# Optimization experiments

Hardware: AMD Instinct MI355X
Metric: run time of the kernel (lower is better)

The kernel has to match this reference:

```python
import jax, jax.numpy as jnp
import numpy as np

BS, NQ, DIM, HEADS, POINTS, LEVELS = 2, 4096, 768, 6, 4, 1
HD = DIM // HEADS
H = W = 64
NV = H * W
EPS = 1e-6


def setup_inputs() -> dict:
    key = jax.random.key(0)
    ks = jax.random.split(key, 16)
    s = 0.02  # param init scale
    return {
        "query": jax.random.normal(ks[0], (BS, NQ, DIM), jnp.float32),
        "reference_points": jax.random.uniform(ks[1], (BS, NQ, LEVELS, 2), jnp.float32),
        "feat": jax.random.normal(ks[2], (BS, NV, DIM), jnp.float32),
        "spatial_shapes": np.array([[H, W]], dtype=np.int64),
        "level_start_index": np.array([0], dtype=np.int64),
        "ln_w": jnp.ones((DIM,), jnp.float32),
        "ln_b": jnp.zeros((DIM,), jnp.float32),
        "vp_w": jax.random.normal(ks[3], (DIM, DIM), jnp.float32) * s,
        "vp_b": jnp.zeros((DIM,), jnp.float32),
        "off_w": jax.random.normal(ks[4], (DIM, HEADS * LEVELS * POINTS * 2), jnp.float32) * s,
        "off_b": jax.random.normal(ks[5], (HEADS * LEVELS * POINTS * 2,), jnp.float32),
        "aw_w": jax.random.normal(ks[6], (DIM, HEADS * LEVELS * POINTS), jnp.float32) * s,
        "aw_b": jnp.zeros((HEADS * LEVELS * POINTS,), jnp.float32),
        "out_w": jax.random.normal(ks[7], (DIM, DIM), jnp.float32) * s,
        "out_b": jnp.zeros((DIM,), jnp.float32),
        "gamma": jax.random.normal(ks[8], (DIM,), jnp.float32) * 0.1,
    }


def _layernorm(x, w, b):
    mu = jnp.mean(x, axis=-1, keepdims=True)
    var = jnp.mean(jnp.square(x - mu), axis=-1, keepdims=True)
    return (x - mu) * jax.lax.rsqrt(var + EPS) * w + b


def _bilinear_sample(img, loc):
    # img: (bs, heads, H, W, hd); loc: (bs, nq, heads, points, 2) in [0,1]
    # matches torch.grid_sample(align_corners=False, padding_mode='zeros')
    bs, heads, h, w, hd = img.shape
    x = loc[..., 0] * w - 0.5
    y = loc[..., 1] * h - 0.5
    x0 = jnp.floor(x)
    y0 = jnp.floor(y)
    wx = x - x0
    wy = y - y0
    x0i = x0.astype(jnp.int32)
    y0i = y0.astype(jnp.int32)
    bi = jnp.arange(bs)[:, None, None, None]
    hi = jnp.arange(heads)[None, None, :, None]

    def gather(yi, xi):
        valid = (xi >= 0) & (xi < w) & (yi >= 0) & (yi < h)
        v = img[bi, hi, jnp.clip(yi, 0, h - 1), jnp.clip(xi, 0, w - 1)]
        return v * valid[..., None].astype(img.dtype)

    v00 = gather(y0i, x0i)
    v01 = gather(y0i, x0i + 1)
    v10 = gather(y0i + 1, x0i)
    v11 = gather(y0i + 1, x0i + 1)
    wx = wx[..., None]
    wy = wy[..., None]
    return (v00 * (1 - wy) * (1 - wx) + v01 * (1 - wy) * wx
            + v10 * wy * (1 - wx) + v11 * wy * wx)


def _msda(q, value, reference_points, spatial_shapes, off_w, off_b, aw_w, aw_b, out_w, out_b):
    bs, nq, _ = q.shape
    nv = value.shape[1]
    value = value.reshape(bs, nv, HEADS, HD)
    offsets = (q @ off_w + off_b).reshape(bs, nq, HEADS, LEVELS, POINTS, 2)
    aw = jax.nn.softmax(q @ aw_w + aw_b, axis=-1).reshape(bs, nq, HEADS, LEVELS, POINTS)
    # offset_normalizer = [W_l, H_l] per level
    norm = jnp.asarray(np.asarray(spatial_shapes)[:, ::-1], jnp.float32)  # (L, 2)
    loc = reference_points[:, :, None, :, None, :] + offsets / norm[None, None, None, :, None, :]
    # loc: (bs, nq, heads, levels, points, 2)
    out = jnp.zeros((bs, nq, HEADS, HD), jnp.float32)
    start = 0
    for l in range(LEVELS):
        h_l, w_l = int(spatial_shapes[l][0]), int(spatial_shapes[l][1])
        img = value[:, start:start + h_l * w_l].reshape(bs, h_l, w_l, HEADS, HD).transpose(0, 3, 1, 2, 4)
        sampled = _bilinear_sample(img, loc[:, :, :, l])  # (bs, nq, heads, points, hd)
        out = out + jnp.einsum('bnhpd,bnhp->bnhd', sampled, aw[:, :, :, l])
        start += h_l * w_l
    return out.reshape(bs, nq, DIM) @ out_w + out_b


def reference(query, reference_points, feat, spatial_shapes, level_start_index,
              ln_w, ln_b, vp_w, vp_b, off_w, off_b, aw_w, aw_b, out_w, out_b, gamma):
    q = _layernorm(query, ln_w, ln_b)
    value = feat @ vp_w + vp_b
    attn = _msda(q, value, reference_points, spatial_shapes,
                 off_w, off_b, aw_w, aw_b, out_w, out_b)
    # identity = zeros, dropout = 0 -> attn as-is; residual scale by gamma
    return query + gamma * attn
```

## Files before the change

kernel.cpp:

```cpp
#include <hip/hip_runtime.h>
#include <hip/hip_bf16.h>
#include <math.h>

#define BSZ 2
#define NQ 4096
#define DIM 768
#define HEADS 6
#define POINTS 4
#define HD 128
#define HW_DIM 64
#define NV (HW_DIM*HW_DIM)
#define M_TOTAL (BSZ*NQ)
#define KDIM 768
#define KSPLIT 2
#define KPART (KDIM/KSPLIT)

#define BM 64
#define BN 128
#define BKK 64
#define NBLK_M (M_TOTAL/BM)
#define NBLK_N (DIM/BN)
#define GEMM_GRID (NBLK_M*NBLK_N)
#define LN_BLOCKS (M_TOTAL/4)
#define TR_BLOCKS (576+576+72)
#define SMALL_BLOCKS (128*KSPLIT)

#define A_TILE (BM*BKK)
#define B_TILE (BN*BKK)
#define SMEM_U16 (2*(A_TILE+B_TILE))

typedef __attribute__((ext_vector_type(8))) short bf16x8;
typedef __attribute__((ext_vector_type(4))) float f32x4;
typedef unsigned int u32;
typedef unsigned short u16;

__device__ inline u16 f2bf(float f) {
    union { float f; u32 u; } v; v.f = f;
    u32 r = v.u + 0x7fffu + ((v.u >> 16) & 1u);
    return (u16)(r >> 16);
}

#define GLD16(g, l) __builtin_amdgcn_global_load_lds( \
    (const __attribute__((address_space(1))) u32*)(g), \
    (__attribute__((address_space(3))) u32*)(l), 16, 0, 0)

__global__ __launch_bounds__(256) void prep_kernel(
        const float* __restrict__ x, const float* __restrict__ lnw,
        const float* __restrict__ lnb, u16* __restrict__ q,
        const float* __restrict__ feat, u16* __restrict__ feat_bf,
        const float* __restrict__ vp_w,  u16* __restrict__ vp_wt,
        const float* __restrict__ out_w, u16* __restrict__ out_wt,
        const float* __restrict__ off_w, const float* __restrict__ aw_w,
        u16* __restrict__ oaw_wt) {
    int b = blockIdx.x;
    if (b < LN_BLOCKS) {
        int wave = threadIdx.x >> 6, lane = threadIdx.x & 63;
        int row = b * 4 + wave;
        int c = lane * 4;
        const float* xr = x + (size_t)row * DIM;
        const float* fr = feat + (size_t)row * DIM;
        float4 v0 = *(const float4*)(xr + c);
        float4 v1 = *(const float4*)(xr + c + 256);
        float4 v2 = *(const float4*)(xr + c + 512);
        float4 f0 = *(const float4*)(fr + c);
        float4 f1 = *(const float4*)(fr + c + 256);
        float4 f2 = *(const float4*)(fr + c + 512);
        u16* fb = feat_bf + (size_t)row * DIM;
        ushort4 fo;
        fo.x = f2bf(f0.x); fo.y = f2bf(f0.y); fo.z = f2bf(f0.z); fo.w = f2bf(f0.w);
        *(ushort4*)(fb + c) = fo;
        fo.x = f2bf(f1.x); fo.y = f2bf(f1.y); fo.z = f2bf(f1.z); fo.w = f2bf(f1.w);
        *(ushort4*)(fb + c + 256) = fo;
        fo.x = f2bf(f2.x); fo.y = f2bf(f2.y); fo.z = f2bf(f2.z); fo.w = f2bf(f2.w);
        *(ushort4*)(fb + c + 512) = fo;

        float s  = v0.x+v0.y+v0.z+v0.w + v1.x+v1.y+v1.z+v1.w + v2.x+v2.y+v2.z+v2.w;
        float ss = v0.x*v0.x+v0.y*v0.y+v0.z*v0.z+v0.w*v0.w
                 + v1.x*v1.x+v1.y*v1.y+v1.z*v1.z+v1.w*v1.w
                 + v2.x*v2.x+v2.y*v2.y+v2.z*v2.z+v2.w*v2.w;
        #pragma unroll
        for (int st = 1; st < 64; st <<= 1) {
            s  += __shfl_xor(s,  st, 64);
            ss += __shfl_xor(ss, st, 64);
        }
        float mean = s * (1.0f / DIM);
        float var  = ss * (1.0f / DIM) - mean * mean;
        float rstd = rsqrtf(var + 1e-6f);
        u16* qr = q + (size_t)row * DIM;
        #pragma unroll
        for (int g = 0; g < 3; g++) {
            float4 v = (g == 0) ? v0 : (g == 1) ? v1 : v2;
            int cc = c + g * 256;
            const float4 ww = *(const float4*)(lnw + cc);
            const float4 bb = *(const float4*)(lnb + cc);
            ushort4 o;
            o.x = f2bf((v.x - mean) * rstd * ww.x + bb.x);
            o.y = f2bf((v.y - mean) * rstd * ww.y + bb.y);
            o.z = f2bf((v.z - mean) * rstd * ww.z + bb.z);
            o.w = f2bf((v.w - mean) * rstd * ww.w + bb.w);
            *(ushort4*)(qr + cc) = o;
        }
    } else {
        int t = b - LN_BLOCKS;
        int z, xk, yk;
        if (t < 576)      { z = 0; xk = t % 24; yk = t / 24; }
        else if (t < 1152){ z = 1; t -= 576; xk = t % 24; yk = t / 24; }
        else              { z = 2; t -= 1152; xk = t % 3; yk = t / 3; }
        __shared__ float tile[32][33];
        int n0 = xk * 32, k0 = yk * 32;
        int tx = threadIdx.x & 31, ty = threadIdx.x >> 5;
        const float* src = (z == 0) ? vp_w : (z == 1) ? out_w : nullptr;
        u16* dst = (z == 0) ? vp_wt : (z == 1) ? out_wt : oaw_wt;
        #pragma unroll
        for (int r = 0; r < 4; r++) {
            int k = k0 + ty + r * 8, n = n0 + tx;
            float v = 0.0f;
            if (z < 2) {
                v = src[(size_t)k * DIM + n];
            } else {
                if (n < 48) v = off_w[(size_t)k * 48 + n];
                else if (n < 72) v = aw_w[(size_t)k * 24 + (n - 48)];
            }
            tile[ty + r * 8][tx] = v;
        }
        __syncthreads();
        #pragma unroll
        for (int r = 0; r < 4; r++) {
            int nn = ty + r * 8, kk = tx;
            int drow = n0 + nn;
            if (z == 2 && drow >= 80) continue;
            dst[(size_t)drow * KDIM + k0 + kk] = f2bf(tile[kk][nn]);
        }
    }
}

__device__ __forceinline__ void gemm_big_body(int b, u16* __restrict__ smem,
        const u16* __restrict__ A, const u16* __restrict__ Bt,
        const float* __restrict__ bias, void* __restrict__ Cout,
        int storeBF16, const float* __restrict__ resid,
        const float* __restrict__ gamma) {
    u16* As = smem;
    u16* Bs = smem + 2 * A_TILE;
    int tid = threadIdx.x, w = tid >> 6, lane = tid & 63;
    int lm = lane & 15, quad = lane >> 4;
    int xcd = b & 7, idx = b >> 3;
    int mb = xcd * 16 + idx / NBLK_N;
    int nb = idx % NBLK_N;
    int m0 = mb * BM, n0 = nb * BN;
    int wr = w & 1, wc = w >> 1;

    int srow = lane >> 3;
    int scol = (lane & 7) ^ srow;
    const u16* Ab = A + (size_t)m0 * KDIM;
    const u16* Bb = Bt + (size_t)n0 * KDIM;

    f32x4 acc[2][4];
    #pragma unroll
    for (int i = 0; i < 2; i++)
        #pragma unroll
        for (int j = 0; j < 4; j++) acc[i][j] = (f32x4){0.f, 0.f, 0.f, 0.f};

    int aoff[2][2], boff[4][2];
    #pragma unroll
    for (int i = 0; i < 2; i++) {
        int row = wr * 32 + i * 16 + lm;
        #pragma unroll
        for (int kk = 0; kk < 2; kk++)
            aoff[i][kk] = row * BKK + (((quad + 4 * kk) ^ (row & 7)) << 3);
    }
    #pragma unroll
    for (int j = 0; j < 4; j++) {
        int row = wc * 64 + j * 16 + lm;
        #pragma unroll
        for (int kk = 0; kk < 2; kk++)
            boff[j][kk] = row * BKK + (((quad + 4 * kk) ^ (row & 7)) << 3);
    }

    auto stage = [&](int buf, int k0) {
        #pragma unroll
        for (int r = 0; r < 2; r++) {
            int row = r * 32 + w * 8 + srow;
            GLD16(Ab + (size_t)row * KDIM + k0 + scol * 8,
                  As + buf * A_TILE + (r * 32 + w * 8) * BKK);
        }
        #pragma unroll
        for (int r = 0; r < 4; r++) {
            int row = r * 32 + w * 8 + srow;
            GLD16(Bb + (size_t)row * KDIM + k0 + scol * 8,
                  Bs + buf * B_TILE + (r * 32 + w * 8) * BKK);
        }
    };

    stage(0, 0);
    __syncthreads();
    const int NT = KDIM / BKK;
    for (int t = 0; t < NT; t++) {
        if (t + 1 < NT) stage((t + 1) & 1, (t + 1) * BKK);
        const u16* Ap = As + (t & 1) * A_TILE;
        const u16* Bp = Bs + (t & 1) * B_TILE;
        #pragma unroll
        for (int kk = 0; kk < 2; kk++) {
            bf16x8 af[2], bf[4];
            #pragma unroll
            for (int i = 0; i < 2; i++) af[i] = *(const bf16x8*)(Ap + aoff[i][kk]);
            #pragma unroll
            for (int j = 0; j < 4; j++) bf[j] = *(const bf16x8*)(Bp + boff[j][kk]);
            #pragma unroll
            for (int i = 0; i < 2; i++)
                #pragma unroll
                for (int j = 0; j < 4; j++)
                    acc[i][j] = __builtin_amdgcn_mfma_f32_16x16x32_bf16(af[i], bf[j], acc[i][j], 0, 0, 0);
        }
        __syncthreads();
    }

    #pragma unroll
    for (int j = 0; j < 4; j++) {
        int col = n0 + wc * 64 + j * 16 + lm;
        float bb = bias[col];
        #pragma unroll
        for (int i = 0; i < 2; i++) {
            #pragma unroll
            for (int r = 0; r < 4; r++) {
                int row = m0 + wr * 32 + i * 16 + quad * 4 + r;
                size_t idxo = (size_t)row * DIM + col;
                float v = acc[i][j][r] + bb;
                if (storeBF16) {
                    ((u16*)Cout)[idxo] = f2bf(v);
                } else {
                    ((float*)Cout)[idxo] = resid[idxo] + gamma[col] * v;
                }
            }
        }
    }
}

#define SA_TILE (64*32)
#define SB_TILE (80*32)
__device__ __forceinline__ void gemm_small_body(int mblk, int part,
        u16* __restrict__ smem,
        const u16* __restrict__ A, const u16* __restrict__ Bt,
        const float* __restrict__ b0, const float* __restrict__ b1,
        float* __restrict__ C) {
    u16* As2 = smem;
    u16* Bs2 = smem + 2 * SA_TILE;
    int tid = threadIdx.x, wave = tid >> 6, lane = tid & 63;
    int lm = lane & 15, quad = lane >> 4;
    int m0 = mblk * 64;
    int kbase = part * KPART;
    f32x4 acc[5];
    #pragma unroll
    for (int i = 0; i < 5; i++) acc[i] = (f32x4){0.f, 0.f, 0.f, 0.f};
    int lrow = lane >> 2, lcol = (lane & 3) * 8;

    auto stage = [&](int buf, int k0) {
        for (int c = wave; c < 9; c += 4) {
            if (c < 4) {
                GLD16(A + (size_t)(m0 + c * 16 + lrow) * KDIM + k0 + lcol,
                      As2 + buf * SA_TILE + c * 16 * 32);
            } else {
                GLD16(Bt + (size_t)((c - 4) * 16 + lrow) * KDIM + k0 + lcol,
                      Bs2 + buf * SB_TILE + (c - 4) * 16 * 32);
            }
        }
    };

    stage(0, kbase);
    __syncthreads();
    const int NT = KPART / 32;
    for (int t = 0; t < NT; t++) {
        if (t + 1 < NT) stage((t + 1) & 1, kbase + (t + 1) * 32);
        const u16* Ap = As2 + (t & 1) * SA_TILE;
        const u16* Bp = Bs2 + (t & 1) * SB_TILE;
        bf16x8 af = *(const bf16x8*)(Ap + (wave * 16 + lm) * 32 + quad * 8);
        #pragma unroll
        for (int bn = 0; bn < 5; bn++) {
            bf16x8 bv = *(const bf16x8*)(Bp + (bn * 16 + lm) * 32 + quad * 8);
            acc[bn] = __builtin_amdgcn_mfma_f32_16x16x32_bf16(af, bv, acc[bn], 0, 0, 0);
        }
        __syncthreads();
    }
    float* Cp = C + (size_t)part * M_TOTAL * 80;
    #pragma unroll
    for (int bn = 0; bn < 5; bn++) {
        int col = bn * 16 + lm;
        float bb = 0.0f;
        if (part == 0) bb = (col < 48) ? b0[col] : ((col < 72) ? b1[col - 48] : 0.0f);
        #pragma unroll
        for (int r = 0; r < 4; r++) {
            int row = m0 + wave * 16 + quad * 4 + r;
            Cp[(size_t)row * 80 + col] = acc[bn][r] + bb;
        }
    }
}

__global__ __launch_bounds__(256, 3) void gemms_kernel(
        const u16* __restrict__ feat_bf, const u16* __restrict__ vp_wt,
        const float* __restrict__ vp_b, u16* __restrict__ v_bf,
        const u16* __restrict__ q_bf, const u16* __restrict__ oaw_wt,
        const float* __restrict__ off_b, const float* __restrict__ aw_b,
        float* __restrict__ oa) {
    __shared__ __align__(16) u16 smem[SMEM_U16];
    int b = blockIdx.x;
    if (b < SMALL_BLOCKS) {
        gemm_small_body(b & 127, b >> 7, smem, q_bf, oaw_wt, off_b, aw_b, oa);
    } else {
        gemm_big_body(b - SMALL_BLOCKS, smem, feat_bf, vp_wt, vp_b, v_bf, 1,
                      nullptr, nullptr);
    }
}

__global__ __launch_bounds__(256, 3) void outgemm_kernel(
        const u16* __restrict__ s_bf, const u16* __restrict__ out_wt,
        const float* __restrict__ out_b, float* __restrict__ out_f,
        const float* __restrict__ query, const float* __restrict__ gamma) {
    __shared__ __align__(16) u16 smem[SMEM_U16];
    gemm_big_body(blockIdx.x, smem, s_bf, out_wt, out_b, out_f, 0, query, gamma);
}

__global__ __launch_bounds__(192) void sample_kernel(
        const float* __restrict__ oa, const float* __restrict__ refp,
        const u16* __restrict__ v, u16* __restrict__ out) {
    int row = blockIdx.x;
    int b = row >> 12;
    int tid = threadIdx.x;
    __shared__ float s_w[4][24];
    __shared__ int   s_o[4][24];
    __shared__ float s_e[24];
    if (tid < 24) {
        int h = tid >> 2, p = tid & 3;
        float ox = 0.f, oy = 0.f, lg = 0.f;
        #pragma unroll
        for (int part = 0; part < KSPLIT; part++) {
            const float* pp = oa + (size_t)part * M_TOTAL * 80 + (size_t)row * 80;
            ox += pp[h * 8 + p * 2 + 0];
            oy += pp[h * 8 + p * 2 + 1];
            lg += pp[48 + tid];
        }
        float rx = refp[row * 2 + 0], ry = refp[row * 2 + 1];
        float x = (rx + ox * (1.0f / HW_DIM)) * HW_DIM - 0.5f;
        float y = (ry + oy * (1.0f / HW_DIM)) * HW_DIM - 0.5f;
        float fx = floorf(x), fy = floorf(y);
        int x0 = (int)fx, y0 = (int)fy;
        int x1 = x0 + 1, y1 = y0 + 1;
        float wx = x - fx, wy = y - fy;
        float vx0 = (x0 >= 0 && x0 < HW_DIM) ? 1.f : 0.f;
        float vx1 = (x1 >= 0 && x1 < HW_DIM) ? 1.f : 0.f;
        float vy0 = (y0 >= 0 && y0 < HW_DIM) ? 1.f : 0.f;
        float vy1 = (y1 >= 0 && y1 < HW_DIM) ? 1.f : 0.f;
        int xc0 = min(max(x0, 0), HW_DIM - 1), xc1 = min(max(x1, 0), HW_DIM - 1);
        int yc0 = min(max(y0, 0), HW_DIM - 1), yc1 = min(max(y1, 0), HW_DIM - 1);
        int base = b * NV * DIM;
        s_o[0][tid] = base + (yc0 * HW_DIM + xc0) * DIM;
        s_o[1][tid] = base + (yc0 * HW_DIM + xc1) * DIM;
        s_o[2][tid] = base + (yc1 * HW_DIM + xc0) * DIM;
        s_o[3][tid] = base + (yc1 * HW_DIM + xc1) * DIM;
        s_w[0][tid] = (1.f - wy) * (1.f - wx) * vy0 * vx0;
        s_w[1][tid] = (1.f - wy) * wx * vy0 * vx1;
        s_w[2][tid] = wy * (1.f - wx) * vy1 * vx0;
        s_w[3][tid] = wy * wx * vy1 * vx1;
        s_e[tid] = lg;
        float m = s_e[0];
        #pragma unroll
        for (int i = 1; i < 24; i++) m = fmaxf(m, s_e[i]);
        s_e[tid] = expf(lg - m);
    }
    __syncthreads();
    float ssum = 0.0f;
    #pragma unroll
    for (int i = 0; i < 24; i++) ssum += s_e[i];
    float inv = 1.0f / ssum;

    int h = tid >> 5;
    int d4 = (tid & 31) * 4;
    const u16* vb = v + h * HD + d4;
    float a0 = 0.f, a1 = 0.f, a2 = 0.f, a3 = 0.f;
    #pragma unroll
    for (int p = 0; p < 4; p++) {
        int idx = h * 4 + p;
        float aw = s_e[idx] * inv;
        #pragma unroll
        for (int c = 0; c < 4; c++) {
            uint2 u = *(const uint2*)(vb + s_o[c][idx]);
            float w = aw * s_w[c][idx];
            a0 += w * __uint_as_float(u.x << 16);
            a1 += w * __uint_as_float(u.x & 0xffff0000u);
            a2 += w * __uint_as_float(u.y << 16);
            a3 += w * __uint_as_float(u.y & 0xffff0000u);
        }
    }
    uint2 pack;
    pack.x = (u32)f2bf(a0) | ((u32)f2bf(a1) << 16);
    pack.y = (u32)f2bf(a2) | ((u32)f2bf(a3) << 16);
    *(uint2*)&out[(size_t)row * DIM + h * HD + d4] = pack;
}

extern "C" void kernel_launch(void* const* d_in, const int* in_sizes, int n_in,
                              void* d_out, int out_size, void* d_ws, size_t ws_size,
                              hipStream_t stream) {
    const float* query = (const float*)d_in[0];
    const float* refp  = (const float*)d_in[1];
    const float* feat  = (const float*)d_in[2];
    const float* ln_w  = (const float*)d_in[5];
    const float* ln_b  = (const float*)d_in[6];
    const float* vp_w  = (const float*)d_in[7];
    const float* vp_b  = (const float*)d_in[8];
    const float* off_w = (const float*)d_in[9];
    const float* off_b = (const float*)d_in[10];
    const float* aw_w  = (const float*)d_in[11];
    const float* aw_b  = (const float*)d_in[12];
    const float* out_w = (const float*)d_in[13];
    const float* out_b = (const float*)d_in[14];
    const float* gamma = (const float*)d_in[15];

    const size_t MD = (size_t)M_TOTAL * DIM;
    char* ws = (char*)d_ws;
    u16* q_bf    = (u16*)ws;                 ws += MD * 2;
    u16* feat_bf = (u16*)ws;                 ws += MD * 2;
    u16* v_bf    = (u16*)ws;                 ws += MD * 2;
    u16* s_bf    = (u16*)ws;                 ws += MD * 2;
    u16* vp_wt   = (u16*)ws;                 ws += (size_t)DIM * DIM * 2;
    u16* out_wt  = (u16*)ws;                 ws += (size_t)DIM * DIM * 2;
    u16* oaw_wt  = (u16*)ws;                 ws += (size_t)80 * KDIM * 2;
    float* oa    = (float*)ws;               ws += (size_t)KSPLIT * M_TOTAL * 80 * 4;
    float* out_f = (float*)d_out;

    prep_kernel<<<LN_BLOCKS + TR_BLOCKS, 256, 0, stream>>>(
        query, ln_w, ln_b, q_bf, feat, feat_bf,
        vp_w, vp_wt, out_w, out_wt, off_w, aw_w, oaw_wt);
    gemms_kernel<<<SMALL_BLOCKS + GEMM_GRID, 256, 0, stream>>>(
        feat_bf, vp_wt, vp_b, v_bf, q_bf, oaw_wt, off_b, aw_b, oa);
    sample_kernel<<<M_TOTAL, 192, 0, stream>>>(oa, refp, v_bf, s_bf);
    outgemm_kernel<<<GEMM_GRID, 256, 0, stream>>>(s_bf, out_wt, out_b, out_f, query, gamma);
}
```

Measured before the change: 176.3 us.

## Triple-buffer GEMM K-loop with BK=32 and explicit vmcnt waits

Restructures the big GEMM main loop from double buffering with BK=64 to triple buffering with BK=32. Loads run two stages ahead, and each iteration uses a single barrier gated by explicit s_waitcnt vmcnt counts instead of two __syncthreads. The LDS swizzle is reworked for the 4-slot rows, and launch bounds rise to 4 blocks per CU. The aim is to hide global-to-LDS latency and cut barrier overhead, at the cost of more K iterations, each with only half the MFMA work. The small GEMM shares the smem buffer and the BKK macro, which risks side effects there.

```diff
diff --git a/kernel.cpp b/kernel.cpp
--- a/kernel.cpp
+++ b/kernel.cpp
@@ -17,7 +17,7 @@
 
 #define BM 64
 #define BN 128
-#define BKK 64
+#define BKK 32
 #define NBLK_M (M_TOTAL/BM)
 #define NBLK_N (DIM/BN)
 #define GEMM_GRID (NBLK_M*NBLK_N)
@@ -27,7 +27,7 @@
 
 #define A_TILE (BM*BKK)
 #define B_TILE (BN*BKK)
-#define SMEM_U16 (2*(A_TILE+B_TILE))
+#define SMEM_U16 (3*(A_TILE+B_TILE))
 
 typedef __attribute__((ext_vector_type(8))) short bf16x8;
 typedef __attribute__((ext_vector_type(4))) float f32x4;
@@ -140,7 +140,7 @@
         int storeBF16, const float* __restrict__ resid,
         const float* __restrict__ gamma) {
     u16* As = smem;
-    u16* Bs = smem + 2 * A_TILE;
+    u16* Bs = smem + 3 * A_TILE;
     int tid = threadIdx.x, w = tid >> 6, lane = tid & 63;
     int lm = lane & 15, quad = lane >> 4;
     int xcd = b & 7, idx = b >> 3;
@@ -149,8 +149,8 @@
     int m0 = mb * BM, n0 = nb * BN;
     int wr = w & 1, wc = w >> 1;
 
-    int srow = lane >> 3;
-    int scol = (lane & 7) ^ srow;
+    int srow = lane >> 2;
+    int sslot = lane & 3;
     const u16* Ab = A + (size_t)m0 * KDIM;
     const u16* Bb = Bt + (size_t)n0 * KDIM;
 
@@ -160,58 +160,59 @@
         #pragma unroll
         for (int j = 0; j < 4; j++) acc[i][j] = (f32x4){0.f, 0.f, 0.f, 0.f};
 
-    int aoff[2][2], boff[4][2];
+    int aoff[2], boff[4];
     #pragma unroll
     for (int i = 0; i < 2; i++) {
         int row = wr * 32 + i * 16 + lm;
-        #pragma unroll
-        for (int kk = 0; kk < 2; kk++)
-            aoff[i][kk] = row * BKK + (((quad + 4 * kk) ^ (row & 7)) << 3);
+        aoff[i] = row * BKK + ((quad ^ (row & 3)) << 3);
     }
     #pragma unroll
     for (int j = 0; j < 4; j++) {
         int row = wc * 64 + j * 16 + lm;
-        #pragma unroll
-        for (int kk = 0; kk < 2; kk++)
-            boff[j][kk] = row * BKK + (((quad + 4 * kk) ^ (row & 7)) << 3);
+        boff[j] = row * BKK + ((quad ^ (row & 3)) << 3);
     }
 
     auto stage = [&](int buf, int k0) {
+        {
+            int row = w * 16 + srow;
+            int sc = sslot ^ (row & 3);
+            GLD16(Ab + (size_t)row * KDIM + k0 + sc * 8,
+                  As + buf * A_TILE + (w * 16) * BKK);
+        }
         #pragma unroll
         for (int r = 0; r < 2; r++) {
-            int row = r * 32 + w * 8 + srow;
-            GLD16(Ab + (size_t)row * KDIM + k0 + scol * 8,
-                  As + buf * A_TILE + (r * 32 + w * 8) * BKK);
-        }
-        #pragma unroll
-        for (int r = 0; r < 4; r++) {
-            int row = r * 32 + w * 8 + srow;
-            GLD16(Bb + (size_t)row * KDIM + k0 + scol * 8,
-                  Bs + buf * B_TILE + (r * 32 + w * 8) * BKK);
+            int row = r * 64 + w * 16 + srow;
+            int sc = sslot ^ (row & 3);
+            GLD16(Bb + (size_t)row * KDIM + k0 + sc * 8,
+                  Bs + buf * B_TILE + (r * 64 + w * 16) * BKK);
         }
     };
 
+    const int NT = KDIM / BKK;
     stage(0, 0);
-    __syncthreads();
-    const int NT = KDIM / BKK;
+    stage(1, BKK);
     for (int t = 0; t < NT; t++) {
-        if (t + 1 < NT) stage((t + 1) & 1, (t + 1) * BKK);
-        const u16* Ap = As + (t & 1) * A_TILE;
-        const u16* Bp = Bs + (t & 1) * B_TILE;
-        #pragma unroll
-        for (int kk = 0; kk < 2; kk++) {
-            bf16x8 af[2], bf[4];
+        if (t < NT - 1) {
+            asm volatile("s_waitcnt vmcnt(3) lgkmcnt(0)" ::: "memory");
+        } else {
+            asm volatile("s_waitcnt vmcnt(0) lgkmcnt(0)" ::: "memory");
+        }
+        __builtin_amdgcn_sched_barrier(0);
+        __builtin_amdgcn_s_barrier();
+        __builtin_amdgcn_sched_barrier(0);
+        if (t + 2 < NT) stage((t + 2) % 3, (t + 2) * BKK);
+        const u16* Ap = As + (t % 3) * A_TILE;
+        const u16* Bp = Bs + (t % 3) * B_TILE;
+        bf16x8 af[2], bf[4];
+        #pragma unroll
+        for (int i = 0; i < 2; i++) af[i] = *(const bf16x8*)(Ap + aoff[i]);
+        #pragma unroll
+        for (int j = 0; j < 4; j++) bf[j] = *(const bf16x8*)(Bp + boff[j]);
+        #pragma unroll
+        for (int i = 0; i < 2; i++)
             #pragma unroll
-            for (int i = 0; i < 2; i++) af[i] = *(const bf16x8*)(Ap + aoff[i][kk]);
-            #pragma unroll
-            for (int j = 0; j < 4; j++) bf[j] = *(const bf16x8*)(Bp + boff[j][kk]);
-            #pragma unroll
-            for (int i = 0; i < 2; i++)
-                #pragma unroll
-                for (int j = 0; j < 4; j++)
-                    acc[i][j] = __builtin_amdgcn_mfma_f32_16x16x32_bf16(af[i], bf[j], acc[i][j], 0, 0, 0);
-        }
-        __syncthreads();
+            for (int j = 0; j < 4; j++)
+                acc[i][j] = __builtin_amdgcn_mfma_f32_16x16x32_bf16(af[i], bf[j], acc[i][j], 0, 0, 0);
     }
 
     #pragma unroll
@@ -294,7 +295,7 @@
     }
 }
 
-__global__ __launch_bounds__(256, 3) void gemms_kernel(
+__global__ __launch_bounds__(256, 4) void gemms_kernel(
         const u16* __restrict__ feat_bf, const u16* __restrict__ vp_wt,
         const float* __restrict__ vp_b, u16* __restrict__ v_bf,
         const u16* __restrict__ q_bf, const u16* __restrict__ oaw_wt,
@@ -310,7 +311,7 @@
     }
 }
 
-__global__ __launch_bounds__(256, 3) void outgemm_kernel(
+__global__ __launch_bounds__(256, 4) void outgemm_kernel(
         const u16* __restrict__ s_bf, const u16* __restrict__ out_wt,
         const float* __restrict__ out_b, float* __restrict__ out_f,
         const float* __restrict__ query, const float* __restrict__ gamma) {
```

Result: slower. 185.5 us (+5.2%).
